# Performance work log

Measured on AMD Instinct MI355X. Metric: run time of the kernel, lower is better.

## Reference

```python
import jax, jax.numpy as jnp
import numpy as np

TOP_K = 2
CAP_FACTOR = 1.25
MIN_CAPACITY = 4


def setup_inputs() -> dict:
    key = jax.random.key(0)
    k1, k2, k3, k4 = jax.random.split(key, 4)
    B, T, C, E = 8, 2048, 1024, 8
    x = jax.random.normal(k1, (B, T, C), dtype=jnp.float32)
    w_g = jax.random.normal(k2, (E, C), dtype=jnp.float32) * 0.02   # router gate (Linear, no bias)
    c_fc = jax.random.normal(k3, (E, C, 4 * C), dtype=jnp.float32) * 0.02
    c_proj = jax.random.normal(k4, (E, 4 * C, C), dtype=jnp.float32) * 0.02
    return {"x": x, "w_g": w_g, "c_fc": c_fc, "c_proj": c_proj}


def reference(x, w_g, c_fc, c_proj):
    B, T, C = x.shape
    E = w_g.shape[0]
    N = B * T
    capacity = max(MIN_CAPACITY, int(CAP_FACTOR * N * TOP_K / E))  # 5120, static

    xf = x.reshape(N, C)
    # ---- Router (eval path: no noise, no aux losses) ----
    logits = xf @ w_g.T                                   # [N, E]
    top_logits, top_idx = jax.lax.top_k(logits, TOP_K)    # [N, k]
    router_probs = jax.nn.softmax(top_logits, axis=-1)    # [N, k]

    # position in expert: cumsum over (k-major, token) flattened order
    oh = jax.nn.one_hot(top_idx, E, dtype=jnp.int32)      # [N, k, E]
    oh_t = oh.transpose(1, 0, 2).reshape(TOP_K * N, E)
    pos = jnp.cumsum(oh_t, axis=0).reshape(TOP_K, N, E).transpose(1, 0, 2)  # [N, k, E]
    rank = jnp.sum((pos - 1) * oh, axis=-1)               # [N, k], 0-based slot in expert buffer
    valid = rank < capacity                               # capacity mask
    probs_masked = router_probs * valid.astype(router_probs.dtype)
    rank_c = jnp.clip(rank, 0, capacity - 1)

    # ---- Dispatch: scatter tokens into [E, capacity, C] buffers ----
    contrib = xf[:, None, :] * valid[..., None].astype(xf.dtype)  # [N, k, C]
    buf = jnp.zeros((E, capacity, C), dtype=xf.dtype).at[top_idx, rank_c].add(contrib)

    # ---- Experts: bmm -> ReLU^2 -> bmm ----
    h = jnp.einsum('ecd,edf->ecf', buf, c_fc)             # [E, cap, 4C]
    h = jnp.square(jax.nn.relu(h))
    expert_out = jnp.einsum('ecf,efd->ecd', h, c_proj)    # [E, cap, C]

    # ---- Combine: gather expert outputs back, weight by router probs ----
    gathered = expert_out[top_idx, rank_c]                # [N, k, C]
    out = jnp.sum(gathered * probs_masked[..., None], axis=1)
    return out.reshape(B, T, C)
```

## Files before the change

kernel.cpp:

```cpp
#include <hip/hip_runtime.h>

#define NE 8
#define CAP 5120
#define NT 16384
#define CD 1024
#define FCD 4096

typedef __attribute__((ext_vector_type(8))) short short8;
typedef __attribute__((ext_vector_type(4))) float f32x4;

__device__ __forceinline__ unsigned short f2bf(float f) {
  unsigned int u = __builtin_bit_cast(unsigned int, f);
  u += 0x7FFFu + ((u >> 16) & 1u);
  return (unsigned short)(u >> 16);
}
__device__ __forceinline__ float bf2f(unsigned short u) {
  unsigned int v = ((unsigned int)u) << 16;
  return __builtin_bit_cast(float, v);
}
__device__ __forceinline__ void g2lds16(const unsigned short* g, unsigned short* l) {
  __builtin_amdgcn_global_load_lds(
      (const __attribute__((address_space(1))) unsigned int*)(unsigned long long)g,
      (__attribute__((address_space(3))) unsigned int*)l,
      16, 0, 0);
}

__global__ __launch_bounds__(256) void fill_i32_k(int* __restrict__ p, int v, int n) {
  int i = blockIdx.x * 256 + threadIdx.x;
  if (i < n) p[i] = v;
}
__global__ __launch_bounds__(256) void fill_zero_f32x4_k(float4* __restrict__ p, size_t n4) {
  size_t i = (size_t)blockIdx.x * 256 + threadIdx.x;
  if (i < n4) p[i] = make_float4(0.f, 0.f, 0.f, 0.f);
}

__global__ __launch_bounds__(256) void transpose_bf16_k(
    const float* __restrict__ in, unsigned short* __restrict__ out, int R, int Cc) {
  __shared__ float tile[64][65];
  const size_t esz = (size_t)R * Cc;
  const float* inp = in + (size_t)blockIdx.z * esz;
  unsigned short* outp = out + (size_t)blockIdx.z * esz;
  const int cbase = blockIdx.x * 64, rbase = blockIdx.y * 64;
  const int t = threadIdx.x;
#pragma unroll
  for (int i = 0; i < 4; ++i) {
    int idx = i * 256 + t;
    int r = idx >> 4, c4 = (idx & 15) * 4;
    const float4 v = *reinterpret_cast<const float4*>(inp + (size_t)(rbase + r) * Cc + cbase + c4);
    tile[r][c4 + 0] = v.x; tile[r][c4 + 1] = v.y; tile[r][c4 + 2] = v.z; tile[r][c4 + 3] = v.w;
  }
  __syncthreads();
#pragma unroll
  for (int i = 0; i < 4; ++i) {
    int idx = i * 256 + t;
    int oc = idx >> 4, q = (idx & 15) * 4;
    ushort4 o;
    o.x = f2bf(tile[q + 0][oc]); o.y = f2bf(tile[q + 1][oc]);
    o.z = f2bf(tile[q + 2][oc]); o.w = f2bf(tile[q + 3][oc]);
    *reinterpret_cast<ushort4*>(outp + (size_t)(cbase + oc) * R + rbase + q) = o;
  }
}

__global__ __launch_bounds__(256) void router_k(
    const float* __restrict__ x, const float* __restrict__ wg,
    unsigned short* __restrict__ xb, int* __restrict__ topidx, float* __restrict__ probs) {
  __shared__ float wls[NE * CD];
  const int t = threadIdx.x;
  {
    const float4* w4 = (const float4*)wg;
    float4* l4 = (float4*)wls;
    for (int i = t; i < NE * CD / 4; i += 256) l4[i] = w4[i];
  }
  __syncthreads();
  const int wave = t >> 6, lane = t & 63;
  const int gw = blockIdx.x * 4 + wave;
  const float4* wls4 = (const float4*)wls;
#pragma unroll
  for (int it = 0; it < 2; ++it) {
    const int n = gw * 2 + it;
    const float4* xr4 = (const float4*)(x + (size_t)n * CD);
    ushort4* xb4 = (ushort4*)(xb + (size_t)n * CD);
    double acc[NE] = {0, 0, 0, 0, 0, 0, 0, 0};
#pragma unroll
    for (int j = 0; j < 4; ++j) {
      const int idx = j * 64 + lane;
      const float4 xv = xr4[idx];
      ushort4 o;
      o.x = f2bf(xv.x); o.y = f2bf(xv.y); o.z = f2bf(xv.z); o.w = f2bf(xv.w);
      xb4[idx] = o;
#pragma unroll
      for (int e = 0; e < NE; ++e) {
        const float4 wv = wls4[e * 256 + idx];
        acc[e] += (double)xv.x * (double)wv.x + (double)xv.y * (double)wv.y
                + (double)xv.z * (double)wv.z + (double)xv.w * (double)wv.w;
      }
    }
#pragma unroll
    for (int s = 32; s >= 1; s >>= 1) {
#pragma unroll
      for (int e = 0; e < NE; ++e) acc[e] += __shfl_xor(acc[e], s, 64);
    }
    if (lane == 0) {
      int i1 = 0; double v1 = acc[0];
      for (int e = 1; e < NE; ++e) if (acc[e] > v1) { v1 = acc[e]; i1 = e; }
      int i2 = -1; double v2 = -1e300;
      for (int e = 0; e < NE; ++e) if (e != i1 && acc[e] > v2) { v2 = acc[e]; i2 = e; }
      float p0 = 1.0f / (1.0f + expf((float)(v2 - v1)));
      topidx[n * 2 + 0] = i1; topidx[n * 2 + 1] = i2;
      probs[n * 2 + 0] = p0; probs[n * 2 + 1] = 1.0f - p0;
    }
  }
}

__global__ __launch_bounds__(256) void hist_k(const int* __restrict__ topidx, int* __restrict__ blkhist) {
  __shared__ int h[16];
  const int t = threadIdx.x;
  if (t < 16) h[t] = 0;
  __syncthreads();
  const int n = blockIdx.x * 256 + t;
  atomicAdd(&h[topidx[n * 2 + 0]], 1);
  atomicAdd(&h[8 + topidx[n * 2 + 1]], 1);
  __syncthreads();
  if (t < 16) blkhist[blockIdx.x * 16 + t] = h[t];
}

__global__ void scan_k(const int* __restrict__ blkhist, int* __restrict__ blkoff, int* __restrict__ totals_cnt) {
  const int t = threadIdx.x;
  if (t < 16) {
    int s = 0;
    for (int b = 0; b < 64; ++b) { blkoff[b * 16 + t] = s; s += blkhist[b * 16 + t]; }
    totals_cnt[t] = s;
  }
  __syncthreads();
  if (t < 8) {
    int tot = totals_cnt[t] + totals_cnt[8 + t];
    totals_cnt[16 + t] = tot < CAP ? tot : CAP;
  }
}

__global__ __launch_bounds__(256) void rank_k(
    const int* __restrict__ topidx, const int* __restrict__ blkoff,
    const int* __restrict__ totals_cnt, int* __restrict__ ranks, int* __restrict__ slotmap) {
  __shared__ int wcnt[2][4][8];
  __shared__ int woff[2][4][8];
  const int t = threadIdx.x, wave = t >> 6, lane = t & 63;
  const int n = blockIdx.x * 256 + t;
  const int e1 = topidx[n * 2 + 0], e2 = topidx[n * 2 + 1];
  const unsigned long long lt = (1ull << lane) - 1ull;
  int pre1 = 0, pre2 = 0;
#pragma unroll
  for (int e = 0; e < 8; ++e) {
    unsigned long long m1 = __ballot(e1 == e);
    unsigned long long m2 = __ballot(e2 == e);
    if (e1 == e) pre1 = __popcll(m1 & lt);
    if (e2 == e) pre2 = __popcll(m2 & lt);
    if (lane == 0) { wcnt[0][wave][e] = __popcll(m1); wcnt[1][wave][e] = __popcll(m2); }
  }
  __syncthreads();
  if (t < 16) {
    int k = t >> 3, e = t & 7, s = 0;
    for (int w = 0; w < 4; ++w) { woff[k][w][e] = s; s += wcnt[k][w][e]; }
  }
  __syncthreads();
  int r1 = blkoff[blockIdx.x * 16 + e1] + woff[0][wave][e1] + pre1;
  int r2 = totals_cnt[e2] + blkoff[blockIdx.x * 16 + 8 + e2] + woff[1][wave][e2] + pre2;
  ranks[n * 2 + 0] = (r1 < CAP) ? r1 : -1;
  ranks[n * 2 + 1] = (r2 < CAP) ? r2 : -1;
  if (r1 < CAP) slotmap[e1 * CAP + r1] = n * 2 + 0;
  if (r2 < CAP) slotmap[e2 * CAP + r2] = n * 2 + 1;
}

template <int WM, int WN, int BM, int BN, int KDIM, int NDIM, bool GATHER, bool RELU2>
__global__ __launch_bounds__(WM * WN * 64) void gemm8_k(
    const unsigned short* __restrict__ A, const unsigned short* __restrict__ Bt,
    unsigned short* __restrict__ Out, const int* __restrict__ slotmap,
    const int* __restrict__ cnt, int e_base, int n_le) {
  constexpr int THREADS = WM * WN * 64;
  constexpr int KT = KDIM / 32;
  constexpr int TM = CAP / BM;
  constexpr int TN = NDIM / BN;
  constexpr int M_REP = BM / WM / 16;
  constexpr int N_REP = BN / WN / 16;
  constexpr int MH = M_REP / 2;
  constexpr int ALOADS = BM * 4 / THREADS;
  constexpr int BLOADS = BN * 4 / THREADS;
  static_assert(ALOADS + BLOADS == 4, "vmcnt literal assumes 4 loads/wave/tile");

  __shared__ unsigned short lA[3][BM * 32];
  __shared__ unsigned short lB[3][BN * 32];

  int pref[9];
  int L = 0;
  for (int i = 0; i < n_le; ++i) {
    pref[i] = L;
    int lm = (cnt[e_base + i] + BM - 1) / BM;
    if (lm > TM) lm = TM;
    L += lm;
  }
  const int totalLive = L * TN;
  const int bid = blockIdx.x;
  if (bid >= totalLive) return;
  const int q = totalLive >> 3, r = totalLive & 7;
  const int xcd = bid & 7, lin = bid >> 3;
  const int wid = (xcd < r ? xcd * (q + 1) : r * (q + 1) + (xcd - r) * q) + lin;
  const int pair = wid / TN;
  const int nt = wid % TN;
  int le = n_le - 1;
  for (int i = 1; i < n_le; ++i) if (pair < pref[i]) { le = i - 1; break; }
  const int mt = pair - pref[le];
  const int e = e_base + le;

  const int tid = threadIdx.x;
  const int wave = tid >> 6, lane = tid & 63;
  const int wr = wave / WN, wc = wave % WN;
  const int l15 = lane & 15, l4 = lane >> 4;

  const unsigned short* pA[ALOADS];
  const unsigned short* pB[BLOADS];
#pragma unroll
  for (int j = 0; j < ALOADS; ++j) {
    const int ci = j * THREADS + tid;
    const int row = ci >> 2, cst = ci & 3;
    const int csrc = cst ^ ((row >> 1) & 3);
    size_t grow;
    if (GATHER) {
      const int sv = slotmap[e * CAP + mt * BM + row];
      grow = (size_t)(sv < 0 ? 0 : (sv >> 1));
    } else {
      grow = (size_t)le * CAP + mt * BM + row;
    }
    pA[j] = A + grow * KDIM + csrc * 8;
  }
#pragma unroll
  for (int j = 0; j < BLOADS; ++j) {
    const int ci = j * THREADS + tid;
    const int row = ci >> 2, cst = ci & 3;
    const int csrc = cst ^ ((row >> 1) & 3);
    pB[j] = Bt + ((size_t)le * NDIM + nt * BN + row) * KDIM + csrc * 8;
  }

  const int ksw = (l4 ^ ((l15 >> 1) & 3)) * 8;
  int aOff[M_REP], bOff[N_REP];
#pragma unroll
  for (int m = 0; m < M_REP; ++m)
    aOff[m] = (wr * (BM / WM) + m * 16 + l15) * 32 + ksw;
#pragma unroll
  for (int n = 0; n < N_REP; ++n)
    bOff[n] = (wc * (BN / WN) + n * 16 + l15) * 32 + ksw;

  f32x4 acc[M_REP][N_REP] = {};

#pragma unroll
  for (int kt = 0; kt < 2; ++kt) {
#pragma unroll
    for (int j = 0; j < ALOADS; ++j)
      g2lds16(pA[j] + kt * 32, &lA[kt][(j * THREADS + wave * 64) * 8]);
#pragma unroll
    for (int j = 0; j < BLOADS; ++j)
      g2lds16(pB[j] + kt * 32, &lB[kt][(j * THREADS + wave * 64) * 8]);
  }

  for (int t = 0; t < KT; ++t) {
    if (t < KT - 1) asm volatile("s_waitcnt vmcnt(4)" ::: "memory");
    else            asm volatile("s_waitcnt vmcnt(0)" ::: "memory");
    __builtin_amdgcn_s_barrier();
    asm volatile("" ::: "memory");

    const int s = t % 3, s2 = (t + 2) % 3;
    const unsigned short* sA = &lA[s][0];
    const unsigned short* sB = &lB[s][0];
    const bool pf = (t + 2 < KT);

    short8 aF[MH], bF[N_REP];
#pragma unroll
    for (int m = 0; m < MH; ++m) aF[m] = *(const short8*)(sA + aOff[m]);
#pragma unroll
    for (int n = 0; n < N_REP; ++n) bF[n] = *(const short8*)(sB + bOff[n]);
    if (pf) {
#pragma unroll
      for (int j = 0; j < ALOADS; ++j)
        g2lds16(pA[j] + (t + 2) * 32, &lA[s2][(j * THREADS + wave * 64) * 8]);
    }
    asm volatile("s_waitcnt lgkmcnt(0)" ::: "memory");
    __builtin_amdgcn_sched_barrier(0);
    __builtin_amdgcn_s_setprio(1);
#pragma unroll
    for (int m = 0; m < MH; ++m)
#pragma unroll
      for (int n = 0; n < N_REP; ++n)
        acc[m][n] = __builtin_amdgcn_mfma_f32_16x16x32_bf16(aF[m], bF[n], acc[m][n], 0, 0, 0);
    __builtin_amdgcn_s_setprio(0);

    short8 aG[MH];
#pragma unroll
    for (int m = 0; m < MH; ++m) aG[m] = *(const short8*)(sA + aOff[MH + m]);
    if (pf) {
#pragma unroll
      for (int j = 0; j < BLOADS; ++j)
        g2lds16(pB[j] + (t + 2) * 32, &lB[s2][(j * THREADS + wave * 64) * 8]);
    }
    asm volatile("s_waitcnt lgkmcnt(0)" ::: "memory");
    __builtin_amdgcn_sched_barrier(0);
    __builtin_amdgcn_s_setprio(1);
#pragma unroll
    for (int m = 0; m < MH; ++m)
#pragma unroll
      for (int n = 0; n < N_REP; ++n)
        acc[MH + m][n] = __builtin_amdgcn_mfma_f32_16x16x32_bf16(aG[m], bF[n], acc[MH + m][n], 0, 0, 0);
    __builtin_amdgcn_s_setprio(0);
  }

  const size_t rowb = (size_t)le * CAP + mt * BM + wr * (BM / WM);
  const int colb = nt * BN + wc * (BN / WN);
#pragma unroll
  for (int m = 0; m < M_REP; ++m)
#pragma unroll
    for (int n = 0; n < N_REP; ++n)
#pragma unroll
      for (int rr = 0; rr < 4; ++rr) {
        float v = acc[m][n][rr];
        if (RELU2) { v = fmaxf(v, 0.0f); v = v * v; }
        Out[(rowb + m * 16 + l4 * 4 + rr) * NDIM + colb + n * 16 + l15] = f2bf(v);
      }
}

__global__ __launch_bounds__(256) void combine_k(
    const unsigned short* __restrict__ eo, const int* __restrict__ topidx,
    const float* __restrict__ probs, const int* __restrict__ ranks, float* __restrict__ out) {
  const int n = blockIdx.x, t = threadIdx.x;
  const int c = t * 4;
  const int e1 = topidx[n * 2 + 0], e2 = topidx[n * 2 + 1];
  const int r1 = ranks[n * 2 + 0], r2 = ranks[n * 2 + 1];
  const float p1 = probs[n * 2 + 0], p2 = probs[n * 2 + 1];
  float o0 = 0.f, o1 = 0.f, o2 = 0.f, o3 = 0.f;
  if (r1 >= 0) {
    const ushort4 v = *(const ushort4*)(eo + ((size_t)e1 * CAP + r1) * CD + c);
    o0 += p1 * bf2f(v.x); o1 += p1 * bf2f(v.y); o2 += p1 * bf2f(v.z); o3 += p1 * bf2f(v.w);
  }
  if (r2 >= 0) {
    const ushort4 v = *(const ushort4*)(eo + ((size_t)e2 * CAP + r2) * CD + c);
    o0 += p2 * bf2f(v.x); o1 += p2 * bf2f(v.y); o2 += p2 * bf2f(v.z); o3 += p2 * bf2f(v.w);
  }
  float4 o; o.x = o0; o.y = o1; o.z = o2; o.w = o3;
  *reinterpret_cast<float4*>(out + (size_t)n * CD + c) = o;
}

extern "C" void kernel_launch(void* const* d_in, const int* in_sizes, int n_in,
                              void* d_out, int out_size, void* d_ws, size_t ws_size,
                              hipStream_t stream) {
  const float* x = (const float*)d_in[0];
  const float* wg = (const float*)d_in[1];
  const float* cfc = (const float*)d_in[2];
  const float* cproj = (const float*)d_in[3];
  float* out = (float*)d_out;
  char* ws = (char*)d_ws;
  (void)in_sizes; (void)n_in; (void)out_size;

  const size_t W1SZ = (size_t)FCD * CD * 2;
  const size_t HSZ  = (size_t)CAP * FCD * 2;
  const size_t EOSZ = (size_t)CAP * CD * 2;

  size_t off = 0;
  auto alloc = [&](size_t bytes) { size_t o = off; off = (off + bytes + 255) & ~(size_t)255; return o; };
  unsigned short* XB = (unsigned short*)(ws + alloc((size_t)NT * CD * 2));
  int* TOPIDX  = (int*)(ws + alloc((size_t)NT * 2 * 4));
  float* PROBS = (float*)(ws + alloc((size_t)NT * 2 * 4));
  int* RANKS   = (int*)(ws + alloc((size_t)NT * 2 * 4));
  int* SLOTMAP = (int*)(ws + alloc((size_t)NE * CAP * 4));
  int* BLKHIST = (int*)(ws + alloc(64 * 16 * 4));
  int* BLKOFF  = (int*)(ws + alloc(64 * 16 * 4));
  int* TOTALS  = (int*)(ws + alloc(256));
  const size_t shared_end = off;
  int* CNT = TOTALS + 16;

  size_t woff = shared_end;
  auto walloc = [&](size_t bytes) { size_t o = woff; woff = (woff + bytes + 255) & ~(size_t)255; return o; };
  const size_t oCFCT   = walloc(NE * W1SZ);
  const size_t oCPROJT = walloc(NE * W1SZ);
  const size_t weights_end = woff;

  int EG = 0;
  for (int g = 8; g >= 1; g >>= 1) {
    size_t need = weights_end + NE * EOSZ + 512 + (size_t)g * HSZ + 512;
    if (ws_size >= need) { EG = g; break; }
  }
  if (EG == 0) {
    fill_zero_f32x4_k<<<(NT * CD / 4 + 255) / 256, 256, 0, stream>>>((float4*)out, (size_t)NT * CD / 4);
    return;
  }

  fill_i32_k<<<(NE * CAP + 255) / 256, 256, 0, stream>>>(SLOTMAP, -1, NE * CAP);
  router_k<<<2048, 256, 0, stream>>>(x, wg, XB, TOPIDX, PROBS);
  hist_k<<<64, 256, 0, stream>>>(TOPIDX, BLKHIST);
  scan_k<<<1, 64, 0, stream>>>(BLKHIST, BLKOFF, TOTALS);
  rank_k<<<64, 256, 0, stream>>>(TOPIDX, BLKOFF, TOTALS, RANKS, SLOTMAP);

  unsigned short* CFCT   = (unsigned short*)(ws + oCFCT);
  unsigned short* CPROJT = (unsigned short*)(ws + oCPROJT);
  transpose_bf16_k<<<dim3(FCD / 64, CD / 64, NE), 256, 0, stream>>>(cfc, CFCT, CD, FCD);
  transpose_bf16_k<<<dim3(CD / 64, FCD / 64, NE), 256, 0, stream>>>(cproj, CPROJT, FCD, CD);

  size_t eoff = weights_end;
  auto ealloc = [&](size_t bytes) { size_t o = eoff; eoff = (eoff + bytes + 255) & ~(size_t)255; return o; };
  unsigned short* EO = (unsigned short*)(ws + ealloc(NE * EOSZ));
  unsigned short* H  = (unsigned short*)(ws + ealloc((size_t)EG * HSZ));

  for (int g = 0; g < NE / EG; ++g) {
    const int eb = g * EG;
    gemm8_k<2, 4, 256, 256, CD, FCD, true, true>
        <<<EG * (CAP / 256) * (FCD / 256), 512, 0, stream>>>(
        XB, CFCT + (size_t)eb * FCD * CD, H, SLOTMAP, CNT, eb, EG);
    gemm8_k<2, 2, 128, 128, FCD, CD, false, false>
        <<<EG * (CAP / 128) * (CD / 128), 256, 0, stream>>>(
        H, CPROJT + (size_t)eb * CD * FCD, EO + (size_t)eb * CAP * CD, SLOTMAP, CNT, eb, EG);
  }
  combine_k<<<NT, 256, 0, stream>>>(EO, TOPIDX, PROBS, RANKS, out);
}
```

Before: 922.7 us.

## Add ping-pong pipelined GEMM kernel with K=64 tiles for first expert matmul

Adds a new GEMM kernel for the gathered first expert matmul (c_fc with ReLU^2). It uses 64-wide K tiles and double-buffered LDS, and splits each tile into quarter-blocks so direct global-to-LDS loads for the next stage are interleaved with MFMA on the current one. Explicit vmcnt/lgkmcnt waits, priority raising and barriers order the phases. The tile-mapping logic is pulled into a shared helper. The deeper K tile cuts the number of barriers per K step, but it uses more LDS and raises the risk of pipelining hazards from the hand-set wait counts.

```diff
diff --git a/kernel.cpp b/kernel.cpp
--- a/kernel.cpp
+++ b/kernel.cpp
@@ -170,6 +170,191 @@
   if (r2 < CAP) slotmap[e2 * CAP + r2] = n * 2 + 1;
 }
 
+template <int BM, int TN>
+__device__ __forceinline__ bool map_tile(const int* cnt, int e_base, int n_le,
+                                         int& le, int& mt, int& nt) {
+  constexpr int TM = CAP / BM;
+  int pref[9];
+  int L = 0;
+  for (int i = 0; i < n_le; ++i) {
+    pref[i] = L;
+    int lm = (cnt[e_base + i] + BM - 1) / BM;
+    if (lm > TM) lm = TM;
+    L += lm;
+  }
+  const int totalLive = L * TN;
+  const int bid = blockIdx.x;
+  if (bid >= totalLive) return false;
+  const int q = totalLive >> 3, r = totalLive & 7;
+  const int xcd = bid & 7, lin = bid >> 3;
+  const int wid = (xcd < r ? xcd * (q + 1) : r * (q + 1) + (xcd - r) * q) + lin;
+  const int pair = wid / TN;
+  nt = wid % TN;
+  le = n_le - 1;
+  for (int i = 1; i < n_le; ++i) if (pair < pref[i]) { le = i - 1; break; }
+  mt = pair - pref[le];
+  return true;
+}
+
+template <int BM, int KDIM, int NDIM, bool GATHER, bool RELU2>
+__global__ __launch_bounds__(512) void gemm8p_k(
+    const unsigned short* __restrict__ A, const unsigned short* __restrict__ Bt,
+    unsigned short* __restrict__ Out, const int* __restrict__ slotmap,
+    const int* __restrict__ cnt, int e_base, int n_le) {
+  constexpr int BN = 256;
+  constexpr int KT = KDIM / 64;
+  constexpr int TN = NDIM / BN;
+  constexpr int M_REP = BM / 32;
+  constexpr int QM = M_REP / 2;
+  constexpr int AL = BM / 128;
+  constexpr int BL = 2;
+  constexpr int V = AL + BL;
+
+  __shared__ unsigned short lA[2][BM * 64];
+  __shared__ unsigned short lB[2][BN * 64];
+
+  int le, mt, nt;
+  if (!map_tile<BM, TN>(cnt, e_base, n_le, le, mt, nt)) return;
+  const int e = e_base + le;
+
+  const int tid = threadIdx.x;
+  const int wave = tid >> 6, lane = tid & 63;
+  const int wr = wave >> 2, wc = wave & 3;
+  const int l15 = lane & 15, l4 = lane >> 4;
+
+  const unsigned short* sApt[2][AL];
+  const unsigned short* sBpt[2][BL];
+#pragma unroll
+  for (int h = 0; h < 2; ++h) {
+#pragma unroll
+    for (int j = 0; j < AL; ++j) {
+      const int lc = j * 512 + tid;
+      const int lr = lc >> 3, pc = lc & 7;
+      const int logc = pc ^ (lr & 7);
+      const int rowT = h * (BM / 2) + lr;
+      size_t grow;
+      if (GATHER) {
+        const int sv = slotmap[e * CAP + mt * BM + rowT];
+        grow = (size_t)(sv < 0 ? 0 : (sv >> 1));
+      } else {
+        grow = (size_t)le * CAP + mt * BM + rowT;
+      }
+      sApt[h][j] = A + grow * KDIM + logc * 8;
+    }
+#pragma unroll
+    for (int j = 0; j < BL; ++j) {
+      const int lc = j * 512 + tid;
+      const int lr = lc >> 3, pc = lc & 7;
+      const int logc = pc ^ (lr & 7);
+      sBpt[h][j] = Bt + ((size_t)le * NDIM + nt * BN + h * 128 + lr) * KDIM + logc * 8;
+    }
+  }
+
+#define STAGE_A(sl, h, tt)                                                              \
+  do { _Pragma("unroll") for (int j = 0; j < AL; ++j)                                   \
+    g2lds16(sApt[h][j] + (size_t)(tt) * 64,                                             \
+            &lA[sl][((h) * (BM / 2) * 8 + j * 512 + wave * 64) * 8]); } while (0)
+#define STAGE_B(sl, h, tt)                                                              \
+  do { _Pragma("unroll") for (int j = 0; j < BL; ++j)                                   \
+    g2lds16(sBpt[h][j] + (size_t)(tt) * 64,                                             \
+            &lB[sl][((h) * 128 * 8 + j * 512 + wave * 64) * 8]); } while (0)
+
+  const int kidx0 = ((0 * 4 + l4) ^ (l15 & 7)) * 8;
+  const int kidx1 = ((1 * 4 + l4) ^ (l15 & 7)) * 8;
+
+#define RD_A(mh)                                                                        \
+  do { _Pragma("unroll") for (int m = 0; m < QM; ++m) {                                 \
+    const int row = (mh) * (BM / 2) + wr * (BM / 4) + m * 16 + l15;                     \
+    aF[m][0] = *(const short8*)(bA + row * 64 + kidx0);                                 \
+    aF[m][1] = *(const short8*)(bA + row * 64 + kidx1); } } while (0)
+#define RD_B(nh)                                                                        \
+  do { _Pragma("unroll") for (int n = 0; n < 2; ++n) {                                  \
+    const int row = (nh) * 128 + wc * 32 + n * 16 + l15;                                \
+    bF[n][0] = *(const short8*)(bB + row * 64 + kidx0);                                 \
+    bF[n][1] = *(const short8*)(bB + row * 64 + kidx1); } } while (0)
+#define LGK0()                                                                          \
+  do { asm volatile("s_waitcnt lgkmcnt(0)" ::: "memory");                               \
+       __builtin_amdgcn_sched_barrier(0); } while (0)
+#define MF(mh, nh)                                                                      \
+  do { __builtin_amdgcn_s_setprio(1);                                                   \
+    _Pragma("unroll") for (int m = 0; m < QM; ++m)                                      \
+      _Pragma("unroll") for (int n = 0; n < 2; ++n) {                                   \
+        acc[(mh) * QM + m][(nh) * 2 + n] = __builtin_amdgcn_mfma_f32_16x16x32_bf16(     \
+            aF[m][0], bF[n][0], acc[(mh) * QM + m][(nh) * 2 + n], 0, 0, 0);             \
+        acc[(mh) * QM + m][(nh) * 2 + n] = __builtin_amdgcn_mfma_f32_16x16x32_bf16(     \
+            aF[m][1], bF[n][1], acc[(mh) * QM + m][(nh) * 2 + n], 0, 0, 0); }           \
+    __builtin_amdgcn_s_setprio(0); } while (0)
+#define VMC_V()  do { if constexpr (V == 4) asm volatile("s_waitcnt vmcnt(4)" ::: "memory"); \
+                      else asm volatile("s_waitcnt vmcnt(3)" ::: "memory"); } while (0)
+#define VMC_2()  asm volatile("s_waitcnt vmcnt(2)" ::: "memory")
+#define VMC_0()  asm volatile("s_waitcnt vmcnt(0)" ::: "memory")
+#define BAR()    do { __builtin_amdgcn_s_barrier(); asm volatile("" ::: "memory"); } while (0)
+
+  f32x4 acc[M_REP][4] = {};
+  short8 aF[QM][2], bF[2][2];
+
+  STAGE_A(0, 0, 0); STAGE_B(0, 0, 0); STAGE_A(0, 1, 0); STAGE_B(0, 1, 0);
+  VMC_V();
+  BAR();
+
+  int s = 0;
+  for (int t = 0; t < KT; ++t) {
+    const int s2 = s ^ 1;
+    const unsigned short* bA = &lA[s][0];
+    const unsigned short* bB = &lB[s][0];
+    const bool more = (t + 1 < KT);
+
+    RD_A(0); RD_B(0);
+    if (more) { STAGE_A(s2, 0, t + 1); VMC_V(); } else { VMC_2(); }
+    LGK0();
+    MF(0, 0);
+    BAR();
+    RD_A(1);
+    if (more) { STAGE_B(s2, 0, t + 1); VMC_V(); } else { VMC_0(); }
+    LGK0();
+    MF(1, 0);
+    BAR();
+    RD_B(1);
+    if (more) STAGE_A(s2, 1, t + 1);
+    LGK0();
+    MF(1, 1);
+    RD_A(0);
+    if (more) { STAGE_B(s2, 1, t + 1); VMC_V(); }
+    LGK0();
+    MF(0, 1);
+    if (more) BAR();
+    s = s2;
+  }
+
+  const size_t rowb = (size_t)le * CAP + mt * BM;
+  const int colb = nt * BN;
+#pragma unroll
+  for (int i = 0; i < M_REP; ++i) {
+    const int mh = i / QM, m = i % QM;
+#pragma unroll
+    for (int j = 0; j < 4; ++j) {
+      const int nh = j / 2, n = j % 2;
+#pragma unroll
+      for (int rr = 0; rr < 4; ++rr) {
+        float v = acc[i][j][rr];
+        if (RELU2) { v = fmaxf(v, 0.0f); v = v * v; }
+        const size_t orow = rowb + mh * (BM / 2) + wr * (BM / 4) + m * 16 + l4 * 4 + rr;
+        Out[orow * NDIM + colb + nh * 128 + wc * 32 + n * 16 + l15] = f2bf(v);
+      }
+    }
+  }
+#undef STAGE_A
+#undef STAGE_B
+#undef RD_A
+#undef RD_B
+#undef LGK0
+#undef MF
+#undef VMC_V
+#undef VMC_2
+#undef VMC_0
+#undef BAR
+}
+
 template <int WM, int WN, int BM, int BN, int KDIM, int NDIM, bool GATHER, bool RELU2>
 __global__ __launch_bounds__(WM * WN * 64) void gemm8_k(
     const unsigned short* __restrict__ A, const unsigned short* __restrict__ Bt,
@@ -177,7 +362,6 @@
     const int* __restrict__ cnt, int e_base, int n_le) {
   constexpr int THREADS = WM * WN * 64;
   constexpr int KT = KDIM / 32;
-  constexpr int TM = CAP / BM;
   constexpr int TN = NDIM / BN;
   constexpr int M_REP = BM / WM / 16;
   constexpr int N_REP = BN / WN / 16;
@@ -189,25 +373,8 @@
   __shared__ unsigned short lA[3][BM * 32];
   __shared__ unsigned short lB[3][BN * 32];
 
-  int pref[9];
-  int L = 0;
-  for (int i = 0; i < n_le; ++i) {
-    pref[i] = L;
-    int lm = (cnt[e_base + i] + BM - 1) / BM;
-    if (lm > TM) lm = TM;
-    L += lm;
-  }
-  const int totalLive = L * TN;
-  const int bid = blockIdx.x;
-  if (bid >= totalLive) return;
-  const int q = totalLive >> 3, r = totalLive & 7;
-  const int xcd = bid & 7, lin = bid >> 3;
-  const int wid = (xcd < r ? xcd * (q + 1) : r * (q + 1) + (xcd - r) * q) + lin;
-  const int pair = wid / TN;
-  const int nt = wid % TN;
-  int le = n_le - 1;
-  for (int i = 1; i < n_le; ++i) if (pair < pref[i]) { le = i - 1; break; }
-  const int mt = pair - pref[le];
+  int le, mt, nt;
+  if (!map_tile<BM, TN>(cnt, e_base, n_le, le, mt, nt)) return;
   const int e = e_base + le;
 
   const int tid = threadIdx.x;
@@ -407,7 +574,7 @@
 
   for (int g = 0; g < NE / EG; ++g) {
     const int eb = g * EG;
-    gemm8_k<2, 4, 256, 256, CD, FCD, true, true>
+    gemm8p_k<256, CD, FCD, true, true>
         <<<EG * (CAP / 256) * (FCD / 256), 512, 0, stream>>>(
         XB, CFCT + (size_t)eb * FCD * CD, H, SLOTMAP, CNT, eb, EG);
     gemm8_k<2, 2, 128, 128, FCD, CD, false, false>
```

New measurement: 905.0 us. Within noise of the previous version (-1.9%).
